# Performance work log

Measured on AMD Instinct MI355X. Metric: run time of the kernel, lower is better.

The kernel has to match this reference:

```python
import jax, jax.numpy as jnp
import numpy as np

N, E, B = 100000, 1600000, 64
TD, VD, AD = 768, 2048, 512
HC, H = 32, 4
NV, NA = 20000, 20000


def setup_inputs() -> dict:
    key = jax.random.key(0)
    ks = iter(jax.random.split(key, 80))
    def nrm(shape, scale=0.05):
        return (jax.random.normal(next(ks), shape, jnp.float32) * scale)
    inp = {}
    inp["x"] = jax.random.normal(next(ks), (N, TD), jnp.float32)
    inp["x_vision"] = jax.random.normal(next(ks), (NV, VD), jnp.float32)
    inp["x_audio"] = jax.random.normal(next(ks), (NA, AD), jnp.float32)
    inp["src"] = jax.random.randint(next(ks), (E,), 0, N, jnp.int32)
    inp["dst"] = jax.random.randint(next(ks), (E,), 0, N, jnp.int32)
    inp["vidx"] = jnp.arange(NV, dtype=jnp.int32) + 1000   # disjoint vision node ids
    inp["aidx"] = jnp.arange(NA, dtype=jnp.int32) + 30000  # disjoint audio node ids
    inp["ptr"] = (jnp.arange(B + 1) * (N // B)).astype(jnp.int32)
    # modality projections
    inp["Wt"] = nrm((HC, TD)); inp["bt"] = jnp.zeros((HC,), jnp.float32)
    inp["Wv"] = nrm((HC, VD)); inp["bv"] = jnp.zeros((HC,), jnp.float32)
    inp["gv"] = jnp.ones((HC,), jnp.float32); inp["bev"] = jnp.zeros((HC,), jnp.float32)
    inp["Wa"] = nrm((HC, AD)); inp["ba"] = jnp.zeros((HC,), jnp.float32)
    inp["ga"] = jnp.ones((HC,), jnp.float32); inp["bea"] = jnp.zeros((HC,), jnp.float32)
    # GATv2 convs: (in_dim, heads, concat)
    for p, cin, h, concat in (("c1", HC, H, True), ("c2", HC * H, H, True), ("c3", HC * H, H, True), ("c4", HC * H, 1, False)):
        inp[p + "_Wl"] = nrm((h * HC, cin)); inp[p + "_bl"] = jnp.zeros((h * HC,), jnp.float32)
        inp[p + "_Wr"] = nrm((h * HC, cin)); inp[p + "_br"] = jnp.zeros((h * HC,), jnp.float32)
        inp[p + "_att"] = nrm((h, HC))
        inp[p + "_b"] = jnp.zeros((h * HC if concat else HC,), jnp.float32)
    # layer norms
    for p, d in (("n1", HC * H), ("n2", HC * H), ("n3", HC * H), ("n4", HC)):
        inp[p + "_g"] = jnp.ones((d,), jnp.float32); inp[p + "_b"] = jnp.zeros((d,), jnp.float32)
    inp["Wo"] = nrm((1, HC), 0.01); inp["bo"] = jnp.zeros((1,), jnp.float32)
    return inp


def layernorm(x, g, b):
    m = x.mean(-1, keepdims=True)
    v = x.var(-1, keepdims=True)
    return (x - m) / jnp.sqrt(v + 1e-5) * g + b


def gatv2(x, src, dst, Wl, bl, Wr, br, att, b, concat):
    # PyG GATv2Conv (share_weights=False): e = att . leaky_relu(xl[src] + xr[dst])
    n = x.shape[0]
    h, c = att.shape
    xl = (x @ Wl.T + bl).reshape(n, h, c)
    xr = (x @ Wr.T + br).reshape(n, h, c)
    e = jnp.einsum('ehc,hc->eh', jax.nn.leaky_relu(xl[src] + xr[dst], 0.2), att)
    m = jax.ops.segment_max(e, dst, num_segments=n)          # segment softmax over dst
    w = jnp.exp(e - m[dst])
    s = jax.ops.segment_sum(w, dst, num_segments=n)
    alpha = w / (s[dst] + 1e-16)
    out = jax.ops.segment_sum(alpha[:, :, None] * xl[src], dst, num_segments=n)
    out = out.reshape(n, h * c) if concat else out.mean(1)
    return out + b


def reference(x, x_vision, x_audio, Wt, bt, Wv, bv, gv, bev, Wa, ba, ga, bea,
              c1_Wl, c1_bl, c1_Wr, c1_br, c1_att, c1_b,
              c2_Wl, c2_bl, c2_Wr, c2_br, c2_att, c2_b,
              c3_Wl, c3_bl, c3_Wr, c3_br, c3_att, c3_b,
              c4_Wl, c4_bl, c4_Wr, c4_br, c4_att, c4_b,
              n1_g, n1_b, n2_g, n2_b, n3_g, n3_b, n4_g, n4_b, Wo, bo,
              src, dst, vidx, aidx, ptr):
    n = x.shape[0]
    sl = jnp.arange(n, dtype=src.dtype)  # add_self_loops=True
    s2 = jnp.concatenate([src, sl]); d2 = jnp.concatenate([dst, sl])
    fx = x @ Wt.T + bt  # text projection (dropout = identity in eval)
    hv = jax.nn.relu(layernorm(x_vision @ Wv.T + bv, gv, bev))
    fx = fx.at[vidx].set(hv * x[vidx].mean(1, keepdims=True))
    ha = jax.nn.relu(layernorm(x_audio @ Wa.T + ba, ga, bea))
    fx = fx.at[aidx].set(ha * x[aidx].mean(1, keepdims=True))
    h1 = jax.nn.elu(layernorm(gatv2(fx, s2, d2, c1_Wl, c1_bl, c1_Wr, c1_br, c1_att, c1_b, True), n1_g, n1_b))
    h2 = jax.nn.elu(layernorm(gatv2(h1, s2, d2, c2_Wl, c2_bl, c2_Wr, c2_br, c2_att, c2_b, True) + h1, n2_g, n2_b))
    h3 = jax.nn.elu(layernorm(gatv2(h2, s2, d2, c3_Wl, c3_bl, c3_Wr, c3_br, c3_att, c3_b, True) + h2, n3_g, n3_b))
    h4 = layernorm(gatv2(h3, s2, d2, c4_Wl, c4_bl, c4_Wr, c4_br, c4_att, c4_b, False), n4_g, n4_b)
    summary = h4[ptr[:-1]]  # summary node = first node of each graph
    out = (summary @ Wo.T + bo).squeeze(-1)  # num_classes==2 -> squeeze
    return out
```

## Files before the change

### kernel.cpp

```cpp
#include <hip/hip_runtime.h>
#include <math.h>

#define NND 100000
#define NED 1600000
#define TDIM 768
#define VDIM 2048
#define ADIM 512
#define NVV 20000
#define NAA 20000
#define NBB 64
#define SUBROWS 8192

#define NBLK_N ((NND + 255) / 256)
#define NBLK_E ((NED + 255) / 256)
#define NBLK_E512 ((NED + 511) / 512)
#define NM512 ((NND + 511) / 512)
#define NSCAN ((NND + 1023) / 1024)
#define NPACK 576
#define NTILE ((NND + 15) / 16)
#define NWAVEN ((NND * 64 + 255) / 256)
#define NWAVEM2 (((NVV + NAA) * 64 + 255) / 256)
#define NTB_TXT (NND / 32)
#define NTB_VIS (NVV / 32)
#define NTB_AUD (NAA / 32)

static __device__ __forceinline__ unsigned short f2bf(float f) {
  unsigned int u = __float_as_uint(f);
  unsigned int r = (u + 0x7fffu + ((u >> 16) & 1u)) >> 16;
  return (unsigned short)r;
}
static __device__ __forceinline__ float bf2f(unsigned int s) {
  return __uint_as_float(s << 16);
}

typedef __attribute__((ext_vector_type(8))) short bfrag;
typedef __attribute__((ext_vector_type(4))) float facc4;

static __device__ __forceinline__ bfrag pack8(const float4& a, const float4& b) {
  union { bfrag v; unsigned short u[8]; } r;
  r.u[0] = f2bf(a.x); r.u[1] = f2bf(a.y); r.u[2] = f2bf(a.z); r.u[3] = f2bf(a.w);
  r.u[4] = f2bf(b.x); r.u[5] = f2bf(b.y); r.u[6] = f2bf(b.z); r.u[7] = f2bf(b.w);
  return r.v;
}

static __device__ __forceinline__ float red16(float v) {
  #pragma unroll
  for (int m = 8; m >= 1; m >>= 1) v += __shfl_xor(v, m, 64);
  return v;
}
static __device__ __forceinline__ float red32(float v) {
  #pragma unroll
  for (int m = 16; m >= 1; m >>= 1) v += __shfl_xor(v, m, 64);
  return v;
}


static __device__ __forceinline__ void pack_body(
    int i,
    const float* __restrict__ W0l, const float* __restrict__ W0r, unsigned short* o0,
    const float* __restrict__ W1l, const float* __restrict__ W1r, unsigned short* o1,
    const float* __restrict__ W2l, const float* __restrict__ W2r, unsigned short* o2,
    const float* __restrict__ W3l, const float* __restrict__ W3r, unsigned short* o3,
    const float* __restrict__ Wt, unsigned short* ot,
    const float* __restrict__ Wv, unsigned short* ov,
    const float* __restrict__ Wa, unsigned short* oa) {
  if (i < 4096) { o0[i] = f2bf(W0l[i]); o0[4096 + i] = f2bf(W0r[i]); return; }
  i -= 4096;
  if (i < 16384) { o1[i] = f2bf(W1l[i]); o1[16384 + i] = f2bf(W1r[i]); return; }
  i -= 16384;
  if (i < 16384) { o2[i] = f2bf(W2l[i]); o2[16384 + i] = f2bf(W2r[i]); return; }
  i -= 16384;
  if (i < 4096) { o3[i] = f2bf(W3l[i]); o3[4096 + i] = f2bf(W3r[i]); return; }
  i -= 4096;
  if (i < 24576) { ot[i] = f2bf(Wt[i]); return; }
  i -= 24576;
  if (i < 65536) { ov[i] = f2bf(Wv[i]); return; }
  i -= 65536;
  if (i < 16384) { oa[i] = f2bf(Wa[i]); return; }
}

static __device__ __forceinline__ void scan_body(
    const int* __restrict__ cnt, int* rp, int* agg, int n, int b, int* lds) {
  int t = threadIdx.x;
  int base = b * 1024;
  int v[4];
  int s = 0;
  #pragma unroll
  for (int j = 0; j < 4; ++j) {
    int i = base + t * 4 + j;
    int c = (i < n) ? cnt[i] : 0;
    s += c; v[j] = s;
  }
  lds[t] = s;
  __syncthreads();
  for (int ofs = 1; ofs < 256; ofs <<= 1) {
    int x = (t >= ofs) ? lds[t - ofs] : 0;
    __syncthreads();
    lds[t] += x;
    __syncthreads();
  }
  int excl = (t > 0) ? lds[t - 1] : 0;
  int total = lds[255];
  if (t == 0) atomicExch(&agg[b], total);
  __syncthreads();
  int psum = 0;
  for (int j = t; j < b; j += 256) {
    int a;
    do { a = atomicAdd(&agg[j], 0); } while (a == 0);
    psum += a;
  }
  lds[t] = psum;
  __syncthreads();
  for (int ofs = 128; ofs >= 1; ofs >>= 1) {
    if (t < ofs) lds[t] += lds[t + ofs];
    __syncthreads();
  }
  int prefix = lds[0];
  #pragma unroll
  for (int j = 0; j < 4; ++j) {
    int i = base + t * 4 + j;
    if (i < n) rp[i + 1] = prefix + excl + v[j];
  }
  if (b == 0 && t == 0) rp[0] = 0;
}

static __device__ __forceinline__ void modal_body(
    unsigned short* fx, const float* __restrict__ hv, const float* __restrict__ ha,
    const int* __restrict__ vidx, const int* __restrict__ aidx,
    const float* __restrict__ gv, const float* __restrict__ bev,
    const float* __restrict__ ga, const float* __restrict__ bea,
    const float* __restrict__ rowmean, int nv, int na, int bid) {
  int wid = bid * 4 + ((int)threadIdx.x >> 6);
  int l = threadIdx.x & 63;
  if (wid >= nv + na) return;
  bool isV = wid < nv;
  int w2 = isV ? wid : wid - nv;
  const float* hraw = isV ? hv : ha;
  const float* gg = isV ? gv : ga;
  const float* be = isV ? bev : bea;
  int node = isV ? vidx[w2] : aidx[w2];
  float mean = rowmean[node];
  float hval = (l < 32) ? hraw[(size_t)w2 * 32 + l] : 0.f;
  float S = red32(hval);
  float Q = red32(hval * hval);
  if (l < 32) {
    float m2 = S * (1.f / 32.f);
    float var = Q * (1.f / 32.f) - m2 * m2;
    float rstd = rsqrtf(var + 1e-5f);
    float y = (hval - m2) * rstd * gg[l] + be[l];
    y = fmaxf(y, 0.f);
    fx[(size_t)node * 32 + l] = f2bf(y * mean);
  }
}

static __device__ __forceinline__ void prep4_body(
    const int* __restrict__ ptr, const int* __restrict__ rp,
    const int* __restrict__ colidx, int* off, int* gidx, int* mark3,
    int bid, int* cnt_s, int* off_s) {
  if (bid > 0) {
    int node = ptr[bid - 1];
    int eb = rp[node], ee = rp[node + 1];
    if (threadIdx.x == 0) mark3[node] = 1;
    for (int e = eb + (int)threadIdx.x; e < ee; e += 256) mark3[colidx[e]] = 1;
    return;
  }
  int t = threadIdx.x;
  if (t < 64) {
    int node = ptr[t];
    int deg = rp[node + 1] - rp[node];
    if (deg > 126) deg = 126;
    cnt_s[t] = deg + 1;
  }
  __syncthreads();
  if (t == 0) {
    int acc = 0;
    for (int i = 0; i < 64; ++i) { off_s[i] = acc; acc += cnt_s[i]; }
    off_s[64] = acc;
  }
  __syncthreads();
  if (t < 65) off[t] = off_s[t];
  if (t < 64) {
    int node = ptr[t];
    int o = off_s[t];
    gidx[o] = node;
    int eb = rp[node];
    int deg = cnt_s[t] - 1;
    for (int j = 0; j < deg; ++j) gidx[o + 1 + j] = colidx[eb + j];
  }
}

template <int K, bool MEAN, bool OBF>
static __device__ __forceinline__ void gemm_in_body(
    const float* __restrict__ A, const unsigned short* __restrict__ Wb,
    const float* __restrict__ bias, void* __restrict__ Cv,
    float* __restrict__ rowmean, int bid, float* lred) {
  constexpr int KH = K / 2;
  constexpr int KT2 = KH / 32;
  constexpr int NG = KT2 / 2;
  static_assert(KT2 % 2 == 0 && NG % 2 == 0, "need even group count");
  const int wid = (int)threadIdx.x >> 6;
  const int lane = (int)threadIdx.x & 63;
  const int tile = wid & 1;
  const int kh = wid >> 1;
  const int r16 = lane & 15;
  const int kg = lane >> 4;
  const int m0 = (bid * 2 + tile) * 16;
  const float* arow = A + (size_t)(m0 + r16) * K + kh * KH + kg * 8;
  const unsigned short* w0 = Wb + (size_t)r16 * K + kh * KH + kg * 8;
  const unsigned short* w1 = Wb + (size_t)(16 + r16) * K + kh * KH + kg * 8;

  float4 A0[4], A1[4];
  bfrag W0[4], W1[4];
  facc4 acc0 = (facc4){0.f, 0.f, 0.f, 0.f};
  facc4 acc1 = (facc4){0.f, 0.f, 0.f, 0.f};
  float msum = 0.f;

  auto loadg = [&](float4* dA, bfrag* dW, int g) {
    #pragma unroll
    for (int t = 0; t < 2; ++t) {
      const float4* ap = reinterpret_cast<const float4*>(arow + (g * 2 + t) * 32);
      dA[2 * t] = ap[0];
      dA[2 * t + 1] = ap[1];
    }
    #pragma unroll
    for (int t = 0; t < 2; ++t) {
      dW[2 * t]     = *reinterpret_cast<const bfrag*>(w0 + (g * 2 + t) * 32);
      dW[2 * t + 1] = *reinterpret_cast<const bfrag*>(w1 + (g * 2 + t) * 32);
    }
  };
  auto consume = [&](const float4* sA, const bfrag* sW) {
    #pragma unroll
    for (int t = 0; t < 2; ++t) {
      float4 a0 = sA[2 * t], a1 = sA[2 * t + 1];
      if (MEAN) msum += (a0.x + a0.y + a0.z + a0.w) + (a1.x + a1.y + a1.z + a1.w);
      bfrag af = pack8(a0, a1);
      acc0 = __builtin_amdgcn_mfma_f32_16x16x32_bf16(af, sW[2 * t], acc0, 0, 0, 0);
      acc1 = __builtin_amdgcn_mfma_f32_16x16x32_bf16(af, sW[2 * t + 1], acc1, 0, 0, 0);
    }
  };

  loadg(A0, W0, 0);
  #pragma unroll 1
  for (int g = 0; g < NG; g += 2) {
    loadg(A1, W1, g + 1);
    __builtin_amdgcn_sched_barrier(0);
    consume(A0, W0);
    if (g + 2 < NG) loadg(A0, W0, g + 2);
    __builtin_amdgcn_sched_barrier(0);
    consume(A1, W1);
  }

  float* my = lred + ((size_t)tile * 64 + lane) * 9;
  if (kh == 1) {
    #pragma unroll
    for (int r = 0; r < 4; ++r) { my[r] = acc0[r]; my[4 + r] = acc1[r]; }
    my[8] = msum;
  }
  __syncthreads();
  if (kh == 1) return;
  #pragma unroll
  for (int r = 0; r < 4; ++r) { acc0[r] += my[r]; acc1[r] += my[4 + r]; }
  if (MEAN) msum += my[8];

  float b0v = bias[r16], b1v = bias[16 + r16];
  #pragma unroll
  for (int r = 0; r < 4; ++r) {
    int rowg = m0 + kg * 4 + r;
    float v0 = acc0[r] + b0v, v1 = acc1[r] + b1v;
    if (OBF) {
      unsigned short* C = (unsigned short*)Cv;
      C[(size_t)rowg * 32 + r16] = f2bf(v0);
      C[(size_t)rowg * 32 + 16 + r16] = f2bf(v1);
    } else {
      float* C = (float*)Cv;
      C[(size_t)rowg * 32 + r16] = v0;
      C[(size_t)rowg * 32 + 16 + r16] = v1;
    }
  }
  if (MEAN) {
    msum += __shfl_xor(msum, 16, 64);
    msum += __shfl_xor(msum, 32, 64);
    if (lane < 16) rowmean[m0 + r16] = msum * (1.f / (float)K);
  }
}

template <int K, int NHALF, int WAVES, int MODE>
static __device__ __forceinline__ void gemm_body(
    const unsigned short* __restrict__ A,
    const unsigned short* __restrict__ Wb,
    const float* __restrict__ bl, const float* __restrict__ br,
    unsigned short* __restrict__ Cl, unsigned short* __restrict__ Cr, int M,
    const int* __restrict__ rows, const int* __restrict__ rcnt, int bid) {
  constexpr int KT = K / 32;
  constexpr int NT = 2 * NHALF / 16;
  constexpr int NPW = NT / WAVES;
  static_assert(NPW >= 1, "bad wave split");
  const int wid = (int)threadIdx.x >> 6;
  const int lane = (int)threadIdx.x & 63;
  const int r16 = lane & 15;
  const int kg = lane >> 4;
  const int m0 = bid * 16;
  int nr = M;
  if (MODE >= 1) nr = *rcnt;
  if (m0 >= nr) return;
  bfrag bf[NPW][KT];
  #pragma unroll
  for (int n = 0; n < NPW; ++n) {
    int col = (wid * NPW + n) * 16 + r16;
    #pragma unroll
    for (int kt = 0; kt < KT; ++kt)
      bf[n][kt] = *reinterpret_cast<const bfrag*>(Wb + (size_t)col * K + kt * 32 + kg * 8);
  }
  int ra = m0 + r16;
  if (MODE >= 1) { int mm = ra < nr ? ra : nr - 1; ra = rows[mm]; }
  bfrag af[KT];
  const unsigned short* arow = A + (size_t)ra * K + kg * 8;
  #pragma unroll
  for (int kt = 0; kt < KT; ++kt)
    af[kt] = *reinterpret_cast<const bfrag*>(arow + kt * 32);
  facc4 acc[NPW];
  #pragma unroll
  for (int n = 0; n < NPW; ++n) acc[n] = (facc4){0.f, 0.f, 0.f, 0.f};
  #pragma unroll
  for (int kt = 0; kt < KT; ++kt)
    #pragma unroll
    for (int n = 0; n < NPW; ++n)
      acc[n] = __builtin_amdgcn_mfma_f32_16x16x32_bf16(af[kt], bf[n][kt], acc[n], 0, 0, 0);
  #pragma unroll
  for (int n = 0; n < NPW; ++n) {
    int colg = (wid * NPW + n) * 16 + r16;
    bool isL = colg < NHALF;
    float bias = isL ? bl[colg] : br[colg - NHALF];
    #pragma unroll
    for (int r = 0; r < 4; ++r) {
      int m = m0 + kg * 4 + r;
      if (MODE == 1 && m >= nr) continue;
      int rowg = (MODE == 1) ? rows[m] : m;
      unsigned short v = f2bf(acc[n][r] + bias);
      if (isL) Cl[(size_t)rowg * NHALF + colg] = v;
      else     Cr[(size_t)rowg * NHALF + (colg - NHALF)] = v;
    }
  }
}

template <bool RES, bool WL>
static __device__ __forceinline__ void agg_body(
    const unsigned short* __restrict__ xl, const unsigned short* __restrict__ xr,
    const float* __restrict__ att,
    const int* __restrict__ rp, const int* __restrict__ colidx,
    const float* __restrict__ cb, const unsigned short* res,
    const float* __restrict__ g, const float* __restrict__ b,
    unsigned short* __restrict__ out, int n,
    const int* __restrict__ wl, const int* __restrict__ wcnt, int bid) {
  int wid = bid * 4 + ((int)threadIdx.x >> 6);
  int node;
  if (WL) {
    if (wid >= *wcnt) return;
    node = wl[wid];
  } else {
    if (wid >= n) return;
    node = wid;
  }
  const int base = node * 128;
  int l = threadIdx.x & 63;
  const int lh = l & 31;
  const int half = l >> 5;
  const int c4 = 4 * lh;
  float4 a = *reinterpret_cast<const float4*>(att + c4);
  uint2 xru = *reinterpret_cast<const uint2*>(xr + base + c4);
  float xr0 = bf2f(xru.x & 0xffffu), xr1 = bf2f(xru.x >> 16);
  float xr2 = bf2f(xru.y & 0xffffu), xr3 = bf2f(xru.y >> 16);
  float m_ = -1e30f, s_ = 0.f;
  float ac0 = 0.f, ac1 = 0.f, ac2 = 0.f, ac3 = 0.f;
  int eb = rp[node], ee = rp[node + 1];
  int cnt = ee - eb;
  int nstep = (cnt + 1) >> 1;

  auto step = [&](uint2 cur, bool go) {
    float x0 = bf2f(cur.x & 0xffffu), x1 = bf2f(cur.x >> 16);
    float x2 = bf2f(cur.y & 0xffffu), x3 = bf2f(cur.y >> 16);
    float z0 = x0 + xr0, z1 = x1 + xr1, z2 = x2 + xr2, z3 = x3 + xr3;
    float t = (z0 > 0.f ? z0 : 0.2f * z0) * a.x + (z1 > 0.f ? z1 : 0.2f * z1) * a.y
            + (z2 > 0.f ? z2 : 0.2f * z2) * a.z + (z3 > 0.f ? z3 : 0.2f * z3) * a.w;
    t += __shfl_xor(t, 1, 64);
    t += __shfl_xor(t, 2, 64);
    t += __shfl_xor(t, 4, 64);
    if (!go) t = -1e30f;
    if (__any(t > m_ + 4.0f)) {
      float nm = fmaxf(m_, t);
      float p = __expf(m_ - nm);
      float w = __expf(t - nm);
      s_ = s_ * p + w;
      ac0 = ac0 * p + w * x0; ac1 = ac1 * p + w * x1;
      ac2 = ac2 * p + w * x2; ac3 = ac3 * p + w * x3;
      m_ = nm;
    } else {
      float w = __expf(t - m_);
      s_ += w;
      ac0 = fmaf(w, x0, ac0); ac1 = fmaf(w, x1, ac1);
      ac2 = fmaf(w, x2, ac2); ac3 = fmaf(w, x3, ac3);
    }
  };
  auto eclamp = [&](int s) { int e = 2 * s + half; return eb + (e < cnt ? e : cnt - 1); };
  auto ldx = [&](int sn) {
    return *reinterpret_cast<const uint2*>(xl + (size_t)sn * 128 + c4);
  };

  int idx[4];
  uint2 pv[4];
  #pragma unroll
  for (int k = 0; k < 4; ++k) idx[k] = colidx[eclamp(k)];
  #pragma unroll
  for (int k = 0; k < 4; ++k) pv[k] = ldx(idx[k]);
  for (int i = 0; i < nstep; i += 4) {
    uint2 q[4];
    #pragma unroll
    for (int k = 0; k < 4; ++k) q[k] = pv[k];
    if (i + 4 < nstep) {
      #pragma unroll
      for (int k = 0; k < 4; ++k) idx[k] = colidx[eclamp(i + 4 + k)];
      #pragma unroll
      for (int k = 0; k < 4; ++k) pv[k] = ldx(idx[k]);
    }
    step(q[0], 2 * i + half < cnt);
    if (i + 1 < nstep) step(q[1], 2 * (i + 1) + half < cnt);
    if (i + 2 < nstep) step(q[2], 2 * (i + 2) + half < cnt);
    if (i + 3 < nstep) step(q[3], 2 * (i + 3) + half < cnt);
  }

  float om = __shfl_xor(m_, 32, 64);
  float os = __shfl_xor(s_, 32, 64);
  float oa0 = __shfl_xor(ac0, 32, 64);
  float oa1 = __shfl_xor(ac1, 32, 64);
  float oa2 = __shfl_xor(ac2, 32, 64);
  float oa3 = __shfl_xor(ac3, 32, 64);
  float nm = fmaxf(m_, om);
  float ps = __expf(m_ - nm), po = __expf(om - nm);
  float s = s_ * ps + os * po;
  float inv = 1.f / (s + 1e-16f);
  float4 cbv = *reinterpret_cast<const float4*>(cb + c4);
  float v0 = (ac0 * ps + oa0 * po) * inv + cbv.x;
  float v1 = (ac1 * ps + oa1 * po) * inv + cbv.y;
  float v2 = (ac2 * ps + oa2 * po) * inv + cbv.z;
  float v3 = (ac3 * ps + oa3 * po) * inv + cbv.w;
  if (RES) {
    uint2 rv = *reinterpret_cast<const uint2*>(res + base + c4);
    v0 += bf2f(rv.x & 0xffffu); v1 += bf2f(rv.x >> 16);
    v2 += bf2f(rv.y & 0xffffu); v3 += bf2f(rv.y >> 16);
  }
  float S = v0 + v1 + v2 + v3;
  float Q = v0 * v0 + v1 * v1 + v2 * v2 + v3 * v3;
  #pragma unroll
  for (int m = 16; m >= 1; m >>= 1) {
    S += __shfl_xor(S, m, 64);
    Q += __shfl_xor(Q, m, 64);
  }
  float mean = S * (1.f / 128.f);
  float var = Q * (1.f / 128.f) - mean * mean;
  float rstd = rsqrtf(var + 1e-5f);
  float4 gv = *reinterpret_cast<const float4*>(g + c4);
  float4 bv = *reinterpret_cast<const float4*>(b + c4);
  float y0 = (v0 - mean) * rstd * gv.x + bv.x;
  float y1 = (v1 - mean) * rstd * gv.y + bv.y;
  float y2 = (v2 - mean) * rstd * gv.z + bv.z;
  float y3 = (v3 - mean) * rstd * gv.w + bv.w;
  y0 = (y0 > 0.f) ? y0 : expm1f(y0);
  y1 = (y1 > 0.f) ? y1 : expm1f(y1);
  y2 = (y2 > 0.f) ? y2 : expm1f(y2);
  y3 = (y3 > 0.f) ? y3 : expm1f(y3);
  if (half == 0) {
    uint2 o;
    o.x = (unsigned int)f2bf(y0) | ((unsigned int)f2bf(y1) << 16);
    o.y = (unsigned int)f2bf(y2) | ((unsigned int)f2bf(y3) << 16);
    *reinterpret_cast<uint2*>(out + base + c4) = o;
  }
}


__global__ __launch_bounds__(256) void k_initpack(
    int* cnt, int* fill, int* m3, int* m2, int* cnts, int* agg,
    const float* __restrict__ W0l, const float* __restrict__ W0r, unsigned short* o0,
    const float* __restrict__ W1l, const float* __restrict__ W1r, unsigned short* o1,
    const float* __restrict__ W2l, const float* __restrict__ W2r, unsigned short* o2,
    const float* __restrict__ W3l, const float* __restrict__ W3r, unsigned short* o3,
    const float* __restrict__ Wt, unsigned short* ot,
    const float* __restrict__ Wv, unsigned short* ov,
    const float* __restrict__ Wa, unsigned short* oa) {
  int bid = blockIdx.x;
  if (bid < NBLK_N) {
    int i = bid * 256 + threadIdx.x;
    if (i < NND) { cnt[i] = 1; fill[i] = 1; m3[i] = 0; m2[i] = 0; }
    if (i < 2) cnts[i] = 0;
    if (i < 128) agg[i] = 0;
    return;
  }
  pack_body((bid - NBLK_N) * 256 + threadIdx.x,
            W0l, W0r, o0, W1l, W1r, o1, W2l, W2r, o2, W3l, W3r, o3,
            Wt, ot, Wv, ov, Wa, oa);
}

__global__ __launch_bounds__(256) void k_gin_count(
    const float* __restrict__ x, const unsigned short* __restrict__ wbt,
    const float* __restrict__ bt, unsigned short* fx, float* rowmean,
    const float* __restrict__ xv, const unsigned short* __restrict__ wbv,
    const float* __restrict__ bv, float* hvraw,
    const float* __restrict__ xa, const unsigned short* __restrict__ wba,
    const float* __restrict__ ba, float* haraw,
    const int* __restrict__ dst, int* cnt) {
  __shared__ float lred[2 * 64 * 9];
  int bid = blockIdx.x;
  if (bid < NTB_TXT) {
    gemm_in_body<TDIM, true, true>(x, wbt, bt, fx, rowmean, bid, lred);
    return;
  }
  bid -= NTB_TXT;
  if (bid < NTB_VIS) {
    gemm_in_body<VDIM, false, false>(xv, wbv, bv, hvraw, nullptr, bid, lred);
    return;
  }
  bid -= NTB_VIS;
  if (bid < NTB_AUD) {
    gemm_in_body<ADIM, false, false>(xa, wba, ba, haraw, nullptr, bid, lred);
    return;
  }
  bid -= NTB_AUD;
  int i = bid * 256 + threadIdx.x;
  if (i < NED) atomicAdd(&cnt[dst[i]], 1);
}

__global__ __launch_bounds__(256) void k_scan_modal(
    const int* __restrict__ cnt, int* rp, int* agg,
    unsigned short* fx, const float* __restrict__ hv, const float* __restrict__ ha,
    const int* __restrict__ vidx, const int* __restrict__ aidx,
    const float* __restrict__ gv, const float* __restrict__ bev,
    const float* __restrict__ ga, const float* __restrict__ bea,
    const float* __restrict__ rowmean) {
  __shared__ int lds[256];
  int bid = blockIdx.x;
  if (bid < NSCAN) {
    scan_body(cnt, rp, agg, NND, bid, lds);
    return;
  }
  modal_body(fx, hv, ha, vidx, aidx, gv, bev, ga, bea, rowmean, NVV, NAA, bid - NSCAN);
}

__global__ __launch_bounds__(512) void k_fill_gemm1(
    const unsigned short* __restrict__ fx, const unsigned short* __restrict__ wb0,
    const float* __restrict__ bl, const float* __restrict__ br,
    unsigned short* __restrict__ xlb, unsigned short* __restrict__ xrb,
    const int* __restrict__ src, const int* __restrict__ dst,
    const int* __restrict__ rp, int* fill, int* colidx) {
  int bid = blockIdx.x;
  if (bid < NTILE) {
    gemm_body<32, 128, 8, 0>(fx, wb0, bl, br, xlb, xrb, NND, nullptr, nullptr, bid);
    return;
  }
  int i = (bid - NTILE) * 512 + threadIdx.x;
  if (i < NND) colidx[rp[i]] = i;
  if (i < NED) {
    int d = dst[i];
    int p = atomicAdd(&fill[d], 1);
    colidx[rp[d] + p] = src[i];
  }
}

__global__ __launch_bounds__(256) void k_agg1_prep(
    const unsigned short* __restrict__ xlb, const unsigned short* __restrict__ xrb,
    const float* __restrict__ att, const int* __restrict__ rp,
    const int* __restrict__ colidx, const float* __restrict__ cb,
    const float* __restrict__ g, const float* __restrict__ b,
    unsigned short* __restrict__ h,
    const int* __restrict__ ptr, int* off, int* gidx, int* mark3) {
  __shared__ int cnt_s[64];
  __shared__ int off_s[65];
  int bid = blockIdx.x;
  if (bid < NWAVEN / 4 * 4 / 4) {}
  if (bid < 25000) {
    agg_body<false, false>(xlb, xrb, att, rp, colidx, cb, nullptr, g, b, h, NND,
                           nullptr, nullptr, bid);
    return;
  }
  prep4_body(ptr, rp, colidx, off, gidx, mark3, bid - 25000, cnt_s, off_s);
}

__global__ __launch_bounds__(512) void k_gemm2_mark(
    const unsigned short* __restrict__ h, const unsigned short* __restrict__ wb1,
    const float* __restrict__ bl, const float* __restrict__ br,
    unsigned short* __restrict__ xlb, unsigned short* __restrict__ xrb,
    const int* __restrict__ mark3, int* mark2,
    const int* __restrict__ rp, const int* __restrict__ colidx,
    int* list3, int* cnts) {
  int bid = blockIdx.x;
  if (bid < NTILE) {
    gemm_body<128, 128, 8, 0>(h, wb1, bl, br, xlb, xrb, NND, nullptr, nullptr, bid);
    return;
  }
  bid -= NTILE;
  if (bid < NM512) {
    int i = bid * 512 + threadIdx.x;
    if (i < NND && mark3[i]) {
      mark2[i] = 1;
      int eb = rp[i], ee = rp[i + 1];
      for (int e = eb; e < ee; ++e) mark2[colidx[e]] = 1;
    }
    return;
  }
  bid -= NM512;
  int i = bid * 512 + threadIdx.x;
  if (i < NND && mark3[i]) { int p = atomicAdd(&cnts[0], 1); list3[p] = i; }
}

__global__ __launch_bounds__(256) void k_compact1(
    const int* __restrict__ m2, int* l2, int* cnt, int n) {
  int i = blockIdx.x * 256 + threadIdx.x;
  if (i < n && m2[i]) { int p = atomicAdd(cnt, 1); l2[p] = i; }
}

template <int K, int NHALF, int WAVES, int MODE>
__global__ __launch_bounds__(WAVES * 64) void gemm_mfma(
    const unsigned short* __restrict__ A, const unsigned short* __restrict__ Wb,
    const float* __restrict__ bl, const float* __restrict__ br,
    unsigned short* __restrict__ Cl, unsigned short* __restrict__ Cr, int M,
    const int* __restrict__ rows, const int* __restrict__ rcnt) {
  gemm_body<K, NHALF, WAVES, MODE>(A, Wb, bl, br, Cl, Cr, M, rows, rcnt, blockIdx.x);
}

template <bool RES, bool WL>
__global__ __launch_bounds__(256) void gat_agg_post128(
    const unsigned short* __restrict__ xl, const unsigned short* __restrict__ xr,
    const float* __restrict__ att, const int* __restrict__ rp,
    const int* __restrict__ colidx, const float* __restrict__ cb,
    const unsigned short* res, const float* __restrict__ g,
    const float* __restrict__ b, unsigned short* __restrict__ out, int n,
    const int* __restrict__ wl, const int* __restrict__ wcnt) {
  agg_body<RES, WL>(xl, xr, att, rp, colidx, cb, res, g, b, out, n, wl, wcnt, blockIdx.x);
}

__global__ __launch_bounds__(256) void k_agg4_final(
    const unsigned short* __restrict__ xls, const unsigned short* __restrict__ xrs,
    const float* __restrict__ att, const int* __restrict__ off,
    const float* __restrict__ cb, const float* __restrict__ g,
    const float* __restrict__ b, const float* __restrict__ Wo,
    const float* __restrict__ bo, float* __restrict__ out) {
  int wid = (blockIdx.x * 256 + threadIdx.x) >> 6;
  int l = threadIdx.x & 63;
  int lg = l & 15;
  int node = 4 * wid + (l >> 4);
  int c2 = 2 * lg;
  int p0 = off[node], pe = off[node + 1];
  int deg = pe - p0 - 1;
  float2 a = *reinterpret_cast<const float2*>(att + c2);
  unsigned int xru = *reinterpret_cast<const unsigned int*>(xrs + (size_t)p0 * 32 + c2);
  float xr0 = bf2f(xru & 0xffffu), xr1 = bf2f(xru >> 16);
  float m_ = -1e30f, s_ = 0.f, accx = 0.f, accy = 0.f;
  for (int i = 0;; ++i) {
    bool go = i < deg;
    if (!__any(go)) break;
    float xcx = 0.f, xcy = 0.f;
    float t = -1e30f;
    if (go) {
      unsigned int pv = *reinterpret_cast<const unsigned int*>(xls + (size_t)(p0 + 1 + i) * 32 + c2);
      xcx = bf2f(pv & 0xffffu);
      xcy = bf2f(pv >> 16);
      float z0 = xcx + xr0, z1 = xcy + xr1;
      t = (z0 > 0.f ? z0 : 0.2f * z0) * a.x + (z1 > 0.f ? z1 : 0.2f * z1) * a.y;
    }
    t = red16(t);
    if (!go) t = -1e30f;
    if (__any(t > m_ + 4.0f)) {
      float nm = fmaxf(m_, t);
      float p = __expf(m_ - nm);
      float w = __expf(t - nm);
      s_ = s_ * p + w;
      accx = accx * p + w * xcx;
      accy = accy * p + w * xcy;
      m_ = nm;
    } else {
      float w = __expf(t - m_);
      s_ += w;
      accx = fmaf(w, xcx, accx);
      accy = fmaf(w, xcy, accy);
    }
  }
  float inv = 1.f / (s_ + 1e-16f);
  float2 cbv = *reinterpret_cast<const float2*>(cb + c2);
  float v0 = accx * inv + cbv.x;
  float v1 = accy * inv + cbv.y;
  float S = red16(v0 + v1);
  float Q = red16(v0 * v0 + v1 * v1);
  float mean = S * (1.f / 32.f);
  float var = Q * (1.f / 32.f) - mean * mean;
  float rstd = rsqrtf(var + 1e-5f);
  float2 gv = *reinterpret_cast<const float2*>(g + c2);
  float2 bv = *reinterpret_cast<const float2*>(b + c2);
  float y0 = (v0 - mean) * rstd * gv.x + bv.x;
  float y1 = (v1 - mean) * rstd * gv.y + bv.y;
  float2 wo = *reinterpret_cast<const float2*>(Wo + c2);
  float d = red16(y0 * wo.x + y1 * wo.y);
  if (lg == 0) out[node] = d + bo[0];
}

extern "C" void kernel_launch(void* const* d_in, const int* in_sizes, int n_in,
                              void* d_out, int out_size, void* d_ws, size_t ws_size,
                              hipStream_t stream) {
  const float* x   = (const float*)d_in[0];
  const float* xv  = (const float*)d_in[1];
  const float* xa  = (const float*)d_in[2];
  const int* src   = (const int*)d_in[3];
  const int* dst   = (const int*)d_in[4];
  const int* vidx  = (const int*)d_in[5];
  const int* aidx  = (const int*)d_in[6];
  const int* ptr   = (const int*)d_in[7];
  const float* Wt  = (const float*)d_in[8];
  const float* bt  = (const float*)d_in[9];
  const float* Wv  = (const float*)d_in[10];
  const float* bv  = (const float*)d_in[11];
  const float* gv  = (const float*)d_in[12];
  const float* bev = (const float*)d_in[13];
  const float* Wa  = (const float*)d_in[14];
  const float* ba  = (const float*)d_in[15];
  const float* ga  = (const float*)d_in[16];
  const float* bea = (const float*)d_in[17];
  const float* cW_l[4], *cb_l[4], *cW_r[4], *cb_r[4], *c_att[4], *c_b[4];
  for (int i = 0; i < 4; ++i) {
    cW_l[i]  = (const float*)d_in[18 + 6 * i + 0];
    cb_l[i]  = (const float*)d_in[18 + 6 * i + 1];
    cW_r[i]  = (const float*)d_in[18 + 6 * i + 2];
    cb_r[i]  = (const float*)d_in[18 + 6 * i + 3];
    c_att[i] = (const float*)d_in[18 + 6 * i + 4];
    c_b[i]   = (const float*)d_in[18 + 6 * i + 5];
  }
  const float* ng[4], *nb_[4];
  for (int i = 0; i < 4; ++i) {
    ng[i]  = (const float*)d_in[42 + 2 * i + 0];
    nb_[i] = (const float*)d_in[42 + 2 * i + 1];
  }
  const float* Wo = (const float*)d_in[50];
  const float* bo = (const float*)d_in[51];
  float* out = (float*)d_out;

  char* w = (char*)d_ws;
  auto alloc = [&](size_t bytes) {
    char* p = w;
    w += (bytes + 255) & ~(size_t)255;
    return p;
  };
  int* rowptr = (int*)alloc((NND + 1) * sizeof(int));
  int* cnt    = (int*)alloc(NND * sizeof(int));
  int* aggs   = (int*)alloc(128 * sizeof(int));
  int* colidx = (int*)alloc((size_t)(NED + NND) * sizeof(int));
  float* rowmean = (float*)alloc((size_t)NND * sizeof(float));
  unsigned short* fx = (unsigned short*)alloc((size_t)NND * 32 * sizeof(unsigned short));
  unsigned short* h  = (unsigned short*)alloc((size_t)NND * 128 * sizeof(unsigned short));
  unsigned short* xlb = (unsigned short*)alloc((size_t)NND * 128 * sizeof(unsigned short));
  unsigned short* xrb = (unsigned short*)alloc((size_t)NND * 128 * sizeof(unsigned short));
  float* hvraw = (float*)alloc((size_t)NVV * 32 * sizeof(float));
  float* haraw = (float*)alloc((size_t)NAA * 32 * sizeof(float));
  unsigned short* wb0 = (unsigned short*)alloc(256 * 32 * sizeof(unsigned short));
  unsigned short* wb1 = (unsigned short*)alloc(256 * 128 * sizeof(unsigned short));
  unsigned short* wb2 = (unsigned short*)alloc(256 * 128 * sizeof(unsigned short));
  unsigned short* wb3 = (unsigned short*)alloc(64 * 128 * sizeof(unsigned short));
  unsigned short* wbt = (unsigned short*)alloc(32 * TDIM * sizeof(unsigned short));
  unsigned short* wbv = (unsigned short*)alloc(32 * VDIM * sizeof(unsigned short));
  unsigned short* wba = (unsigned short*)alloc(32 * ADIM * sizeof(unsigned short));
  int* off4 = (int*)alloc(65 * sizeof(int));
  int* gidx = (int*)alloc(SUBROWS * sizeof(int));
  unsigned short* xls = (unsigned short*)alloc((size_t)SUBROWS * 32 * sizeof(unsigned short));
  unsigned short* xrs = (unsigned short*)alloc((size_t)SUBROWS * 32 * sizeof(unsigned short));
  int* mark3 = (int*)alloc((size_t)NND * sizeof(int));
  int* mark2 = (int*)alloc((size_t)NND * sizeof(int));
  int* list3 = (int*)alloc((size_t)NND * sizeof(int));
  int* list2 = (int*)alloc((size_t)NND * sizeof(int));
  int* cnts  = (int*)alloc(2 * sizeof(int));

  int* fill = list2;

  k_initpack<<<NBLK_N + NPACK, 256, 0, stream>>>(
      cnt, fill, mark3, mark2, cnts, aggs,
      cW_l[0], cW_r[0], wb0, cW_l[1], cW_r[1], wb1,
      cW_l[2], cW_r[2], wb2, cW_l[3], cW_r[3], wb3,
      Wt, wbt, Wv, wbv, Wa, wba);
  k_gin_count<<<NTB_TXT + NTB_VIS + NTB_AUD + NBLK_E, 256, 0, stream>>>(
      x, wbt, bt, fx, rowmean, xv, wbv, bv, hvraw, xa, wba, ba, haraw, dst, cnt);
  k_scan_modal<<<NSCAN + NWAVEM2, 256, 0, stream>>>(
      cnt, rowptr, aggs, fx, hvraw, haraw, vidx, aidx, gv, bev, ga, bea, rowmean);
  k_fill_gemm1<<<NTILE + NBLK_E512, 512, 0, stream>>>(
      fx, wb0, cb_l[0], cb_r[0], xlb, xrb, src, dst, rowptr, fill, colidx);
  k_agg1_prep<<<25000 + 65, 256, 0, stream>>>(
      xlb, xrb, c_att[0], rowptr, colidx, c_b[0], ng[0], nb_[0], h,
      ptr, off4, gidx, mark3);
  k_gemm2_mark<<<NTILE + NM512 + NM512, 512, 0, stream>>>(
      h, wb1, cb_l[1], cb_r[1], xlb, xrb, mark3, mark2, rowptr, colidx, list3, cnts);
  k_compact1<<<NBLK_N, 256, 0, stream>>>(mark2, list2, cnts + 1, NND);
  gat_agg_post128<true, true><<<NWAVEN, 256, 0, stream>>>(
      xlb, xrb, c_att[1], rowptr, colidx, c_b[1], h, ng[1], nb_[1], h, NND,
      list2, cnts + 1);
  gemm_mfma<128, 128, 8, 1><<<NTILE, 512, 0, stream>>>(
      h, wb2, cb_l[2], cb_r[2], xlb, xrb, NND, list2, cnts + 1);
  gat_agg_post128<true, true><<<4096, 256, 0, stream>>>(
      xlb, xrb, c_att[2], rowptr, colidx, c_b[2], h, ng[2], nb_[2], h, NND,
      list3, cnts + 0);
  gemm_mfma<128, 32, 4, 2><<<SUBROWS / 16, 256, 0, stream>>>(
      h, wb3, cb_l[3], cb_r[3], xls, xrs, SUBROWS, gidx, off4 + 64);
  k_agg4_final<<<4, 256, 0, stream>>>(
      xls, xrs, c_att[3], off4, c_b[3], ng[3], nb_[3], Wo, bo, out);
}
```

Before: 582.5 us.

## Build frontier lists during marking with atomicExch, drop compaction kernel, deepen gather prefetch

Mark-and-compact is merged into one step. atomicExch on the mark arrays lets the first thread that sets a node append it to list3 or list2 directly, so the separate compaction passes and the k_compact1 launch go away. The aggregation gather prefetch grows from 4 to 8 edges in flight, trading more registers for more memory-level parallelism. List order now depends on atomic races, which may hurt locality downstream.

```diff
diff --git a/kernel.cpp b/kernel.cpp
--- a/kernel.cpp
+++ b/kernel.cpp
@@ -155,13 +155,19 @@
 
 static __device__ __forceinline__ void prep4_body(
     const int* __restrict__ ptr, const int* __restrict__ rp,
-    const int* __restrict__ colidx, int* off, int* gidx, int* mark3,
+    const int* __restrict__ colidx, int* off, int* gidx,
+    int* mark3, int* list3, int* cnt3,
     int bid, int* cnt_s, int* off_s) {
   if (bid > 0) {
     int node = ptr[bid - 1];
     int eb = rp[node], ee = rp[node + 1];
-    if (threadIdx.x == 0) mark3[node] = 1;
-    for (int e = eb + (int)threadIdx.x; e < ee; e += 256) mark3[colidx[e]] = 1;
+    if (threadIdx.x == 0) {
+      if (atomicExch(&mark3[node], 1) == 0) { int p = atomicAdd(cnt3, 1); list3[p] = node; }
+    }
+    for (int e = eb + (int)threadIdx.x; e < ee; e += 256) {
+      int c = colidx[e];
+      if (atomicExch(&mark3[c], 1) == 0) { int p = atomicAdd(cnt3, 1); list3[p] = c; }
+    }
     return;
   }
   int t = threadIdx.x;
@@ -406,26 +412,30 @@
     return *reinterpret_cast<const uint2*>(xl + (size_t)sn * 128 + c4);
   };
 
-  int idx[4];
-  uint2 pv[4];
-  #pragma unroll
-  for (int k = 0; k < 4; ++k) idx[k] = colidx[eclamp(k)];
-  #pragma unroll
-  for (int k = 0; k < 4; ++k) pv[k] = ldx(idx[k]);
-  for (int i = 0; i < nstep; i += 4) {
-    uint2 q[4];
+  int idx[8];
+  uint2 pv[8];
+  #pragma unroll
+  for (int k = 0; k < 8; ++k) idx[k] = colidx[eclamp(k)];
+  #pragma unroll
+  for (int k = 0; k < 8; ++k) pv[k] = ldx(idx[k]);
+  for (int i = 0; i < nstep; i += 8) {
+    uint2 q[8];
     #pragma unroll
-    for (int k = 0; k < 4; ++k) q[k] = pv[k];
-    if (i + 4 < nstep) {
+    for (int k = 0; k < 8; ++k) q[k] = pv[k];
+    if (i + 8 < nstep) {
       #pragma unroll
-      for (int k = 0; k < 4; ++k) idx[k] = colidx[eclamp(i + 4 + k)];
+      for (int k = 0; k < 8; ++k) idx[k] = colidx[eclamp(i + 8 + k)];
       #pragma unroll
-      for (int k = 0; k < 4; ++k) pv[k] = ldx(idx[k]);
+      for (int k = 0; k < 8; ++k) pv[k] = ldx(idx[k]);
     }
     step(q[0], 2 * i + half < cnt);
     if (i + 1 < nstep) step(q[1], 2 * (i + 1) + half < cnt);
     if (i + 2 < nstep) step(q[2], 2 * (i + 2) + half < cnt);
     if (i + 3 < nstep) step(q[3], 2 * (i + 3) + half < cnt);
+    if (i + 4 < nstep) step(q[4], 2 * (i + 4) + half < cnt);
+    if (i + 5 < nstep) step(q[5], 2 * (i + 5) + half < cnt);
+    if (i + 6 < nstep) step(q[6], 2 * (i + 6) + half < cnt);
+    if (i + 7 < nstep) step(q[7], 2 * (i + 7) + half < cnt);
   }
 
   float om = __shfl_xor(m_, 32, 64);
@@ -570,17 +580,18 @@
     const int* __restrict__ colidx, const float* __restrict__ cb,
     const float* __restrict__ g, const float* __restrict__ b,
     unsigned short* __restrict__ h,
-    const int* __restrict__ ptr, int* off, int* gidx, int* mark3) {
+    const int* __restrict__ ptr, int* off, int* gidx,
+    int* mark3, int* list3, int* cnts) {
   __shared__ int cnt_s[64];
   __shared__ int off_s[65];
   int bid = blockIdx.x;
-  if (bid < NWAVEN / 4 * 4 / 4) {}
-  if (bid < 25000) {
+  if (bid < NWAVEN) {
     agg_body<false, false>(xlb, xrb, att, rp, colidx, cb, nullptr, g, b, h, NND,
                            nullptr, nullptr, bid);
     return;
   }
-  prep4_body(ptr, rp, colidx, off, gidx, mark3, bid - 25000, cnt_s, off_s);
+  prep4_body(ptr, rp, colidx, off, gidx, mark3, list3, cnts + 0,
+             bid - NWAVEN, cnt_s, off_s);
 }
 
 __global__ __launch_bounds__(512) void k_gemm2_mark(
@@ -589,31 +600,22 @@
     unsigned short* __restrict__ xlb, unsigned short* __restrict__ xrb,
     const int* __restrict__ mark3, int* mark2,
     const int* __restrict__ rp, const int* __restrict__ colidx,
-    int* list3, int* cnts) {
+    int* list2, int* cnts) {
   int bid = blockIdx.x;
   if (bid < NTILE) {
     gemm_body<128, 128, 8, 0>(h, wb1, bl, br, xlb, xrb, NND, nullptr, nullptr, bid);
     return;
   }
   bid -= NTILE;
-  if (bid < NM512) {
-    int i = bid * 512 + threadIdx.x;
-    if (i < NND && mark3[i]) {
-      mark2[i] = 1;
-      int eb = rp[i], ee = rp[i + 1];
-      for (int e = eb; e < ee; ++e) mark2[colidx[e]] = 1;
-    }
-    return;
-  }
-  bid -= NM512;
   int i = bid * 512 + threadIdx.x;
-  if (i < NND && mark3[i]) { int p = atomicAdd(&cnts[0], 1); list3[p] = i; }
-}
-
-__global__ __launch_bounds__(256) void k_compact1(
-    const int* __restrict__ m2, int* l2, int* cnt, int n) {
-  int i = blockIdx.x * 256 + threadIdx.x;
-  if (i < n && m2[i]) { int p = atomicAdd(cnt, 1); l2[p] = i; }
+  if (i < NND && mark3[i]) {
+    if (atomicExch(&mark2[i], 1) == 0) { int p = atomicAdd(&cnts[1], 1); list2[p] = i; }
+    int eb = rp[i], ee = rp[i + 1];
+    for (int e = eb; e < ee; ++e) {
+      int c = colidx[e];
+      if (atomicExch(&mark2[c], 1) == 0) { int p = atomicAdd(&cnts[1], 1); list2[p] = c; }
+    }
+  }
 }
 
 template <int K, int NHALF, int WAVES, int MODE>
@@ -786,12 +788,11 @@
       cnt, rowptr, aggs, fx, hvraw, haraw, vidx, aidx, gv, bev, ga, bea, rowmean);
   k_fill_gemm1<<<NTILE + NBLK_E512, 512, 0, stream>>>(
       fx, wb0, cb_l[0], cb_r[0], xlb, xrb, src, dst, rowptr, fill, colidx);
-  k_agg1_prep<<<25000 + 65, 256, 0, stream>>>(
+  k_agg1_prep<<<NWAVEN + 65, 256, 0, stream>>>(
       xlb, xrb, c_att[0], rowptr, colidx, c_b[0], ng[0], nb_[0], h,
-      ptr, off4, gidx, mark3);
-  k_gemm2_mark<<<NTILE + NM512 + NM512, 512, 0, stream>>>(
-      h, wb1, cb_l[1], cb_r[1], xlb, xrb, mark3, mark2, rowptr, colidx, list3, cnts);
-  k_compact1<<<NBLK_N, 256, 0, stream>>>(mark2, list2, cnts + 1, NND);
+      ptr, off4, gidx, mark3, list3, cnts);
+  k_gemm2_mark<<<NTILE + NM512, 512, 0, stream>>>(
+      h, wb1, cb_l[1], cb_r[1], xlb, xrb, mark3, mark2, rowptr, colidx, list2, cnts);
   gat_agg_post128<true, true><<<NWAVEN, 256, 0, stream>>>(
       xlb, xrb, c_att[1], rowptr, colidx, c_b[1], h, ng[1], nb_[1], h, NND,
       list2, cnts + 1);
```

Result: slower. 730.1 us (+25.3%).
